# Kernel tuning notes

Hardware: AMD Instinct MI355X
Metric: run time of the kernel (lower is better)

The kernel has to match this reference:

```python
import jax, jax.numpy as jnp
import numpy as np
import math

B, NMAX, PE, E, DS, NF = 8, 128, 64, 5, 64, 8  # E = num_edge_features + 1


def setup_inputs() -> dict:
    key = jax.random.key(0)
    ks = jax.random.split(key, 10)
    total = B * NMAX
    x = jax.random.normal(ks[0], (total, PE), jnp.float32)
    batch = jnp.arange(total, dtype=jnp.int32) // NMAX  # sorted graph ids, full graphs
    q = jax.random.uniform(ks[1], (B,), jnp.float32, 0.1, 0.9)  # keep sin(2*pi*q) away from 0
    s = 0.05
    return dict(
        x=x, batch=batch, q=q,
        w_attn=jax.random.normal(ks[2], (PE, 4 * E * PE), jnp.float32) * s,
        b_attn=jnp.zeros((4 * E * PE,), jnp.float32),
        w_node=jax.random.normal(ks[3], (PE, NF), jnp.float32) * s,
        b_node=jnp.zeros((NF,), jnp.float32),
        w_phi=jax.random.normal(ks[4], (DS,), jnp.float32) * s,   # Linear(1, DS) weight
        b_phi=jax.random.normal(ks[5], (DS,), jnp.float32) * s,
        w_ctx=jax.random.normal(ks[6], (DS, DS), jnp.float32) * s,  # Linear(DS, DS, bias=False)
        w_self=jax.random.normal(ks[7], (DS,), jnp.float32) * s,  # Linear(1, DS) weight
        b_self=jax.random.normal(ks[8], (DS,), jnp.float32) * s,
        w_out=jax.random.normal(ks[9], (DS,), jnp.float32) * s,   # Linear(DS, 1) weight
        b_out=jnp.zeros((), jnp.float32),
    )


def _to_dense(batch, vals, n_graphs, n_max):
    # torch_geometric.to_dense_batch for sorted batch vector
    starts = jnp.searchsorted(batch, jnp.arange(n_graphs, dtype=batch.dtype))
    pos = jnp.arange(batch.shape[0]) - starts[batch]
    dense = jnp.zeros((n_graphs, n_max, vals.shape[-1]), vals.dtype).at[batch, pos].set(vals)
    mask = jnp.zeros((n_graphs, n_max), bool).at[batch, pos].set(True)
    return dense, mask


def reference(x, batch, q, w_attn, b_attn, w_node, b_node,
              w_phi, b_phi, w_ctx, w_self, b_self, w_out, b_out):
    scale = 1.0 / math.sqrt(E * PE)
    x_hat = x @ w_node + b_node                              # (total, NF)
    proj = x @ w_attn + b_attn                               # (total, 4*E*PE)
    dense, mask = _to_dense(batch, proj, B, NMAX)            # (B, N, 4*E*PE), (B, N)
    k1, q1, k2, q2 = jnp.split(dense, 4, axis=-1)
    heads = lambda t: t.reshape(B, NMAX, E, PE).transpose(0, 2, 1, 3)  # (B, E, N, PE)
    k1, q1, k2, q2 = heads(k1), heads(q1), heads(k2), heads(q2)
    z_re = jnp.einsum('bend,bemd->benm', k1, q1) * scale     # (B, E, N, N)
    z_im = jnp.einsum('bend,bemd->benm', k2, q2) * scale
    c = jnp.cos(2.0 * math.pi * q)[:, None, None, None]
    s = jnp.sin(2.0 * math.pi * q)[:, None, None, None]
    z = z_re + z_im * (2.0 - c) / s                          # (B, E, N, N)
    eye = jnp.eye(NMAX, dtype=bool)
    edge_mask = mask[:, :, None] & mask[:, None, :] & ~eye   # (B, N, N)
    # DeepSetClassifier
    zt = z[..., None]                                        # (B, E, N, N, 1)
    phi_out = zt * w_phi + b_phi                             # (B, E, N, N, DS)
    m = edge_mask[:, None, :, :, None].astype(z.dtype)       # (B, 1, N, N, 1)
    denom = jnp.maximum(edge_mask.sum(-1).astype(z.dtype), 1.0)[:, None, :, None]  # (B,1,N,1)
    ctx = (m * phi_out).sum(3) / denom                       # (B, E, N, DS) masked neighbor mean
    h = jax.nn.gelu(zt * w_self + b_self + (ctx @ w_ctx)[:, :, :, None, :],
                    approximate=False)                        # (B, E, N, N, DS)
    e = (h * w_out).sum(-1) + b_out                          # (B, E, N, N)
    e_hat = jnp.transpose(e, (0, 3, 2, 1))                   # transpose(-1, 1) -> (B, N, N, E)
    return (e_hat, x_hat, edge_mask, mask)
```

## Files before the change

kernel.cpp:

```cpp
#include <hip/hip_runtime.h>
#include <hip/hip_bf16.h>

#define NB 8
#define NMAXN 128
#define PEH 64
#define NE 5
#define DSZ 64
#define NFEAT 8
#define TOTALN 1024
#define PCOLS 1280

#define OUT_XHAT (NB*NMAXN*NMAXN*NE)
#define OUT_EM   (OUT_XHAT + TOTALN*NFEAT)
#define OUT_MASK (OUT_EM + NB*NMAXN*NMAXN)


__global__ void k_fused1(const float* __restrict__ x, const float* __restrict__ qv,
                         const float* __restrict__ w_attn, const float* __restrict__ b_attn,
                         const float* __restrict__ w_node, const float* __restrict__ b_node,
                         const float* __restrict__ w_phi, const float* __restrict__ b_phi,
                         const float* __restrict__ w_ctx, const float* __restrict__ b_self,
                         float* __restrict__ ws, float* __restrict__ out,
                         int offZbar, int offWpc, int offC1, int offFac, int doProj)
{
    int blk = blockIdx.x, t = threadIdx.x;
    if (blk < 256) {
        if (!doProj) return;
        __shared__ float xs[4 * 64];
        int r0 = blk * 4;
        if (t < 256) xs[t] = x[r0 * PEH + t];
        __syncthreads();
        float4 b4 = *(const float4*)&b_attn[4 * t];
        float4 a0 = b4, a1 = b4, a2 = b4, a3 = b4;
        const float* wp = w_attn + 4 * t;
        #pragma unroll 4
        for (int k = 0; k < 64; k++) {
            float4 w4 = *(const float4*)&wp[k * PCOLS];
            float x0 = xs[k], x1 = xs[64 + k], x2 = xs[128 + k], x3 = xs[192 + k];
            a0.x = fmaf(x0, w4.x, a0.x); a0.y = fmaf(x0, w4.y, a0.y); a0.z = fmaf(x0, w4.z, a0.z); a0.w = fmaf(x0, w4.w, a0.w);
            a1.x = fmaf(x1, w4.x, a1.x); a1.y = fmaf(x1, w4.y, a1.y); a1.z = fmaf(x1, w4.z, a1.z); a1.w = fmaf(x1, w4.w, a1.w);
            a2.x = fmaf(x2, w4.x, a2.x); a2.y = fmaf(x2, w4.y, a2.y); a2.z = fmaf(x2, w4.z, a2.z); a2.w = fmaf(x2, w4.w, a2.w);
            a3.x = fmaf(x3, w4.x, a3.x); a3.y = fmaf(x3, w4.y, a3.y); a3.z = fmaf(x3, w4.z, a3.z); a3.w = fmaf(x3, w4.w, a3.w);
        }
        float* pr = ws + r0 * PCOLS + 4 * t;
        *(float4*)&pr[0]         = a0;
        *(float4*)&pr[PCOLS]     = a1;
        *(float4*)&pr[2 * PCOLS] = a2;
        *(float4*)&pr[3 * PCOLS] = a3;
        return;
    }
    int b2 = blk - 256;
    if (b2 < 32) {
        if (t < 256) {
            int g = b2 * 256 + t;
            int row = g >> 3, f = g & 7;
            const float* xr = x + row * PEH;
            float acc = b_node[f];
            #pragma unroll 8
            for (int k = 0; k < PEH; k++) acc = fmaf(xr[k], w_node[k * NFEAT + f], acc);
            out[OUT_XHAT + g] = acc;
        }
    } else if (b2 < 48) {
        int base = (b2 - 32) * 8192;
        for (int g = base + t; g < base + 8192; g += 320) {
            int n = (g >> 7) & 127, m = g & 127;
            out[OUT_EM + g] = (n == m) ? 0.0f : 1.0f;
        }
    } else if (b2 == 48) {
        for (int g = t; g < 1024; g += 320) out[OUT_MASK + g] = 1.0f;
    } else if (b2 == 49) {
        if (t < 64) {
            float wpv = 0.f, bpv = 0.f;
            for (int i = 0; i < 64; i++) {
                float wc = w_ctx[i * 64 + t];
                wpv = fmaf(w_phi[i], wc, wpv);
                bpv = fmaf(b_phi[i], wc, bpv);
            }
            ws[offWpc + t] = wpv;
            ws[offC1 + t]  = b_self[t] + bpv;
        } else if (t < 72) {
            int b = t - 64;
            float qq = qv[b];
            float ang = 6.2831853071795864f * qq;
            float c = cosf(ang), s = sinf(ang);
            ws[offFac + b] = (2.0f - c) / s;
        }
    } else {
        int base = (b2 - 50) * 2560;
        for (int g = t; g < 2560; g += 320) ws[offZbar + base + g] = 0.0f;
    }
}

__device__ __forceinline__ void z_store4(float acc[4][4], float* ws, float* zp,
                                         int zsF, int offZbar,
                                         int b, int e, int mq, int t)
{
    int tx = t & 7, ty = t >> 3;
    int m0 = 4 * tx, n0 = 4 * ty;
    __hip_bfloat16* zsb = (__hip_bfloat16*)(ws + zsF);
    float psum[4] = {0.f, 0.f, 0.f, 0.f};
    #pragma unroll
    for (int c = 0; c < 4; c++) {
        int mg = mq * 32 + m0 + c;
        union { ushort4 u; __hip_bfloat16 h[4]; } pk;
        #pragma unroll
        for (int r = 0; r < 4; r++) {
            pk.h[r] = __float2bfloat16(acc[r][c]);
            if (mg != n0 + r) psum[r] += acc[r][c];
        }
        *(ushort4*)&zsb[((b * NMAXN + mg) * NE + e) * NMAXN + n0] = pk.u;
    }
    #pragma unroll
    for (int r = 0; r < 4; r++) zp[(n0 + r) * 8 + tx] = psum[r];
    __syncthreads();
    if (t < 128) {
        float s = 0.f;
        #pragma unroll
        for (int xx = 0; xx < 8; xx++) s += zp[t * 8 + xx];
        atomicAdd(&ws[offZbar + (b * NE + e) * NMAXN + t], s);
    }
}

__global__ void k_z_fast(float* __restrict__ ws, int zsF, int offZbar, int offFac)
{
    __shared__ alignas(16) float sm[8192 + 1280 + 1024];
    float* smA = sm;
    float* smQ = sm + 8192;
    float* zp  = sm + 8192 + 1280;

    int t = threadIdx.x;
    int blk = blockIdx.x;
    int ms = blk & 7, be = blk >> 3;
    int b = be / 5, e = be - 5 * b;
    float fac = ws[offFac + b];
    const float scale = 0.05590169943749474f;
    float sfac = scale * fac;

    const float* proj = ws;
    int kn = t >> 1, kkb = (t & 1) * 32;
    int qm = t & 15, qkb = (t >> 4) * 4;

    int tx = t & 7, ty = t >> 3;
    int m0 = 2 * tx, n0 = 4 * ty;
    float acc[4][2] = {};

    for (int pass = 0; pass < 2; pass++) {
        __syncthreads();
        int colK = (pass ? 640 : 0)   + e * 64;
        int colQ = (pass ? 960 : 320) + e * 64;
        float sc = pass ? sfac : scale;
        const float* prK = proj + (b * NMAXN + kn) * PCOLS + colK + kkb;
        #pragma unroll
        for (int j4 = 0; j4 < 8; j4++) {
            float4 v = *(const float4*)&prK[4 * j4];
            smA[(kkb + 4*j4 + 0) * 128 + kn] = sc * v.x;
            smA[(kkb + 4*j4 + 1) * 128 + kn] = sc * v.y;
            smA[(kkb + 4*j4 + 2) * 128 + kn] = sc * v.z;
            smA[(kkb + 4*j4 + 3) * 128 + kn] = sc * v.w;
        }
        const float* prQ = proj + (b * NMAXN + ms * 16 + qm) * PCOLS + colQ + qkb;
        {
            float4 v = *(const float4*)&prQ[0];
            smQ[(qkb + 0) * 20 + qm] = v.x;
            smQ[(qkb + 1) * 20 + qm] = v.y;
            smQ[(qkb + 2) * 20 + qm] = v.z;
            smQ[(qkb + 3) * 20 + qm] = v.w;
        }
        __syncthreads();
        for (int k = 0; k < 64; k++) {
            float4 a4 = *(const float4*)&smA[k * 128 + n0];
            float2 q2 = *(const float2*)&smQ[k * 20 + m0];
            float ar[4] = {a4.x, a4.y, a4.z, a4.w};
            #pragma unroll
            for (int r = 0; r < 4; r++) {
                acc[r][0] = fmaf(ar[r], q2.x, acc[r][0]);
                acc[r][1] = fmaf(ar[r], q2.y, acc[r][1]);
            }
        }
    }
    __syncthreads();

    __hip_bfloat16* zsb = (__hip_bfloat16*)(ws + zsF);
    float psum[4] = {0.f, 0.f, 0.f, 0.f};
    #pragma unroll
    for (int c = 0; c < 2; c++) {
        int mg = ms * 16 + m0 + c;
        union { ushort4 u; __hip_bfloat16 h[4]; } pk;
        #pragma unroll
        for (int r = 0; r < 4; r++) {
            pk.h[r] = __float2bfloat16(acc[r][c]);
            if (mg != n0 + r) psum[r] += acc[r][c];
        }
        *(ushort4*)&zsb[((b * NMAXN + mg) * NE + e) * NMAXN + n0] = pk.u;
    }
    #pragma unroll
    for (int r = 0; r < 4; r++) zp[(n0 + r) * 8 + tx] = psum[r];
    __syncthreads();
    if (t < 128) {
        float s = 0.f;
        #pragma unroll
        for (int xx = 0; xx < 8; xx++) s += zp[t * 8 + xx];
        atomicAdd(&ws[offZbar + (b * NE + e) * NMAXN + t], s);
    }
}

__global__ void k_z_slow(const float* __restrict__ x, const float* __restrict__ w_attn,
                         const float* __restrict__ b_attn, float* __restrict__ ws,
                         int zsF, int offZbar, int offFac)
{
    __shared__ alignas(16) float sm[8320 + 2304 + 1024];
    float* xsm = sm;
    float* smA = sm;
    float* smQ = sm + 8320;
    float* zp  = sm + 8320 + 2304;

    int t = threadIdx.x;
    int blk = blockIdx.x;
    int mq = blk & 3, be = blk >> 2;
    int b = be / 5, e = be - 5 * b;
    float fac = ws[offFac + b];
    const float scale = 0.05590169943749474f;
    float sfac = scale * fac;

    int kn   = t >> 1;
    int kkb  = (t & 1) * 32;
    int qm   = t & 31;
    int qkb  = (t >> 5) * 8;
    int mglo = mq * 32 + qm;

    int tx = t & 7, ty = t >> 3;
    int m0 = 4 * tx, n0 = 4 * ty;
    float acc[4][4] = {};

    for (int pass = 0; pass < 2; pass++) {
        __syncthreads();
        for (int i = t; i < 128 * 16; i += 256) {
            int n = i >> 4, dd = (i & 15) * 4;
            float4 xv = *(const float4*)&x[(b * NMAXN + n) * PEH + dd];
            float* dst = &xsm[n * 65 + dd];
            dst[0] = xv.x; dst[1] = xv.y; dst[2] = xv.z; dst[3] = xv.w;
        }
        __syncthreads();
        int colK = (pass ? 640 : 0)   + e * 64 + kkb;
        int colQ = (pass ? 960 : 320) + e * 64 + qkb;
        float rk[32], rq[8];
        #pragma unroll
        for (int j = 0; j < 32; j++) rk[j] = b_attn[colK + j];
        #pragma unroll
        for (int j = 0; j < 8; j++)  rq[j] = b_attn[colQ + j];
        for (int d = 0; d < 64; d++) {
            const float* wrow = w_attn + d * PCOLS;
            float xk = xsm[kn * 65 + d];
            float xq = xsm[mglo * 65 + d];
            #pragma unroll
            for (int j4 = 0; j4 < 8; j4++) {
                float4 w4 = *(const float4*)&wrow[colK + 4 * j4];
                rk[4*j4+0] = fmaf(xk, w4.x, rk[4*j4+0]);
                rk[4*j4+1] = fmaf(xk, w4.y, rk[4*j4+1]);
                rk[4*j4+2] = fmaf(xk, w4.z, rk[4*j4+2]);
                rk[4*j4+3] = fmaf(xk, w4.w, rk[4*j4+3]);
            }
            #pragma unroll
            for (int j4 = 0; j4 < 2; j4++) {
                float4 w4 = *(const float4*)&wrow[colQ + 4 * j4];
                rq[4*j4+0] = fmaf(xq, w4.x, rq[4*j4+0]);
                rq[4*j4+1] = fmaf(xq, w4.y, rq[4*j4+1]);
                rq[4*j4+2] = fmaf(xq, w4.z, rq[4*j4+2]);
                rq[4*j4+3] = fmaf(xq, w4.w, rq[4*j4+3]);
            }
        }
        __syncthreads();
        float sc = pass ? sfac : scale;
        #pragma unroll
        for (int j = 0; j < 32; j++) smA[(kkb + j) * 128 + kn] = sc * rk[j];
        #pragma unroll
        for (int j = 0; j < 8; j++)  smQ[(qkb + j) * 36 + qm] = rq[j];
        __syncthreads();
        for (int k = 0; k < 64; k++) {
            float4 a4 = *(const float4*)&smA[k * 128 + n0];
            float4 q4 = *(const float4*)&smQ[k * 36 + m0];
            float ar[4] = {a4.x, a4.y, a4.z, a4.w};
            float qr[4] = {q4.x, q4.y, q4.z, q4.w};
            #pragma unroll
            for (int r = 0; r < 4; r++)
                #pragma unroll
                for (int c = 0; c < 4; c++)
                    acc[r][c] = fmaf(ar[r], qr[c], acc[r][c]);
        }
    }
    __syncthreads();
    z_store4(acc, ws, zp, zsF, offZbar, b, e, mq, t);
}

__device__ __forceinline__ float gelu_fast(float x) {
    float x2 = x * x;
    float w  = -1.5957691216057308f * x * fmaf(0.044715f, x2, 1.0f);
    float ew = __expf(w);
    return x * __builtin_amdgcn_rcpf(1.0f + ew);
}

__global__ void k_epi(const float* __restrict__ ws, const float* __restrict__ w_self,
                      const float* __restrict__ w_out, const float* __restrict__ b_out,
                      float* __restrict__ out,
                      int zsF, int offZbar, int offWpc, int offC1)
{
    __shared__ alignas(16) float4 cwi[64];
    int t = threadIdx.x;
    int b = blockIdx.x >> 7, m = blockIdx.x & 127;
    if (t < 64)
        cwi[t] = make_float4(w_self[t], ws[offWpc + t], ws[offC1 + t], w_out[t]);
    float zbv = ws[offZbar + b * 640 + t] * (1.0f / 127.0f);
    __syncthreads();

    const __hip_bfloat16* zsb = (const __hip_bfloat16*)(ws + zsF);
    int e = t >> 7, n = t & 127;
    float zv = __bfloat162float(zsb[(b * NMAXN + m) * 640 + t]);
    float acc = b_out[0];
    #pragma unroll 8
    for (int d = 0; d < 64; d++) {
        float4 c = cwi[d];
        float arg = fmaf(zv, c.x, fmaf(zbv, c.y, c.z));
        acc = fmaf(gelu_fast(arg), c.w, acc);
    }
    out[(b * NMAXN + m) * 640 + n * NE + e] = acc;
}

extern "C" void kernel_launch(void* const* d_in, const int* in_sizes, int n_in,
                              void* d_out, int out_size, void* d_ws, size_t ws_size,
                              hipStream_t stream)
{
    const float* x      = (const float*)d_in[0];
    const float* q      = (const float*)d_in[2];
    const float* w_attn = (const float*)d_in[3];
    const float* b_attn = (const float*)d_in[4];
    const float* w_node = (const float*)d_in[5];
    const float* b_node = (const float*)d_in[6];
    const float* w_phi  = (const float*)d_in[7];
    const float* b_phi  = (const float*)d_in[8];
    const float* w_ctx  = (const float*)d_in[9];
    const float* w_self = (const float*)d_in[10];
    const float* b_self = (const float*)d_in[11];
    const float* w_out  = (const float*)d_in[12];
    const float* b_out  = (const float*)d_in[13];
    float* ws  = (float*)d_ws;
    float* out = (float*)d_out;

    const bool big = ws_size >= (size_t)(1643656 * 4 + 64);
    const int zsF     = big ? (TOTALN * PCOLS) : 0;
    const int offZbar = zsF + 327680;
    const int offWpc  = offZbar + 5120;
    const int offC1   = offWpc + 64;
    const int offFac  = offC1 + 64;

    k_fused1<<<308, 320, 0, stream>>>(x, q, w_attn, b_attn, w_node, b_node,
                                      w_phi, b_phi, w_ctx, b_self,
                                      ws, out, offZbar, offWpc, offC1, offFac, big ? 1 : 0);
    if (big) {
        k_z_fast<<<320, 256, 0, stream>>>(ws, zsF, offZbar, offFac);
    } else {
        k_z_slow<<<160, 256, 0, stream>>>(x, w_attn, b_attn, ws, zsF, offZbar, offFac);
    }
    k_epi<<<1024, 640, 0, stream>>>(ws, w_self, w_out, b_out, out,
                                    zsF, offZbar, offWpc, offC1);
}
```

Measured before the change: 120.6 us.

## Fuse z GEMM with GELU epilogue and compute neighbor sums algebraically

Replaces the z-GEMM kernel and the separate epilogue kernel with two kernels. The first computes each row's masked neighbor sum of z directly from the projections as k·(sum of Q minus own Q), so no atomics or stored z are needed. The second recomputes z tiles in registers and applies the GELU DeepSet epilogue in place, writing e_hat directly. This removes the bf16 z round trip through global memory and one launch. It adds an extra small launch and recomputes K tiles across more blocks.

```diff
diff --git a/kernel.cpp b/kernel.cpp
--- a/kernel.cpp
+++ b/kernel.cpp
@@ -91,6 +91,131 @@
     }
 }
 
+__global__ void k_qsum(float* __restrict__ ws, int offZbar, int offFac)
+{
+    __shared__ float Qs[128];
+    __shared__ float part[256];
+    int t = threadIdx.x, blk = blockIdx.x;
+    int b = blk / 5, e = blk - 5 * b;
+    float fac = ws[offFac + b];
+    const float scale = 0.05590169943749474f;
+    float sfac = scale * fac;
+    const float* proj = ws;
+
+    int grp = t >> 6, k = t & 63;
+    int colQ = ((grp >> 1) ? 960 : 320) + e * 64 + k;
+    int m0 = (grp & 1) * 64;
+    float s = 0.f;
+    for (int m = 0; m < 64; m++) s += proj[(b * NMAXN + m0 + m) * PCOLS + colQ];
+    part[t] = s;
+    __syncthreads();
+    if (t < 64)       Qs[t] = part[t] + part[t + 64];
+    else if (t < 128) Qs[t] = part[t + 64] + part[t + 128];
+    __syncthreads();
+
+    int n = t & 127, half = t >> 7;
+    int colK  = (half ? 640 : 0)   + e * 64;
+    int colQ2 = (half ? 960 : 320) + e * 64;
+    const float* rowp = proj + (b * NMAXN + n) * PCOLS;
+    float sc = half ? sfac : scale;
+    float d = 0.f;
+    #pragma unroll 4
+    for (int kk = 0; kk < 64; kk++)
+        d += rowp[colK + kk] * (Qs[half * 64 + kk] - rowp[colQ2 + kk]);
+    part[t] = d * sc;
+    __syncthreads();
+    if (t < 128)
+        ws[offZbar + (b * NE + e) * NMAXN + t] = (part[t] + part[t + 128]) * (1.0f / 127.0f);
+}
+
+__device__ __forceinline__ float gelu_fast(float x) {
+    float x2 = x * x;
+    float w  = -1.5957691216057308f * x * fmaf(0.044715f, x2, 1.0f);
+    float ew = __expf(w);
+    return x * __builtin_amdgcn_rcpf(1.0f + ew);
+}
+
+__global__ void __launch_bounds__(256) k_zepi(float* __restrict__ ws,
+                      const float* __restrict__ w_self, const float* __restrict__ w_out,
+                      const float* __restrict__ b_out, float* __restrict__ out,
+                      int offZbar, int offWpc, int offC1, int offFac)
+{
+    __shared__ alignas(16) float smA[64 * 128];
+    __shared__ alignas(16) float smQ[64 * 12];
+    __shared__ alignas(16) float zbs[128];
+    __shared__ alignas(16) float4 cwi[64];
+
+    int t = threadIdx.x, blk = blockIdx.x;
+    int ms = blk & 15, be = blk >> 4;
+    int b = be / 5, e = be - 5 * b;
+    float fac = ws[offFac + b];
+    const float scale = 0.05590169943749474f;
+    float sfac = scale * fac;
+    const float* proj = ws;
+
+    if (t < 64)  cwi[t] = make_float4(w_self[t], ws[offWpc + t], ws[offC1 + t], w_out[t]);
+    if (t < 128) zbs[t] = ws[offZbar + (b * NE + e) * NMAXN + t];
+
+    int kn = t >> 1, kkb = (t & 1) * 32;
+    int qm = t & 7,  qkb = (t >> 3) * 2;
+    int tx = t & 7,  ty = t >> 3;
+    int n0 = 4 * ty;
+    int mg = ms * 8 + tx;
+    float acc[4] = {0.f, 0.f, 0.f, 0.f};
+
+    for (int pass = 0; pass < 2; pass++) {
+        __syncthreads();
+        int colK = (pass ? 640 : 0)   + e * 64;
+        int colQ = (pass ? 960 : 320) + e * 64;
+        float sc = pass ? sfac : scale;
+        const float* prK = proj + (b * NMAXN + kn) * PCOLS + colK + kkb;
+        #pragma unroll
+        for (int j4 = 0; j4 < 8; j4++) {
+            float4 v = *(const float4*)&prK[4 * j4];
+            smA[(kkb + 4*j4 + 0) * 128 + kn] = sc * v.x;
+            smA[(kkb + 4*j4 + 1) * 128 + kn] = sc * v.y;
+            smA[(kkb + 4*j4 + 2) * 128 + kn] = sc * v.z;
+            smA[(kkb + 4*j4 + 3) * 128 + kn] = sc * v.w;
+        }
+        {
+            float2 v = *(const float2*)&proj[(b * NMAXN + mg) * PCOLS + colQ + qkb];
+            smQ[(qkb + 0) * 12 + qm] = v.x;
+            smQ[(qkb + 1) * 12 + qm] = v.y;
+        }
+        __syncthreads();
+        #pragma unroll 4
+        for (int k = 0; k < 64; k++) {
+            const float4 a4 = *(const float4*)&smA[k * 128 + n0];
+            float qv = smQ[k * 12 + tx];
+            acc[0] = fmaf(a4.x, qv, acc[0]);
+            acc[1] = fmaf(a4.y, qv, acc[1]);
+            acc[2] = fmaf(a4.z, qv, acc[2]);
+            acc[3] = fmaf(a4.w, qv, acc[3]);
+        }
+    }
+
+    float zb0 = zbs[n0], zb1 = zbs[n0 + 1], zb2 = zbs[n0 + 2], zb3 = zbs[n0 + 3];
+    float bo = b_out[0];
+    float e0 = bo, e1 = bo, e2 = bo, e3 = bo;
+    #pragma unroll 4
+    for (int d = 0; d < 64; d++) {
+        float4 c = cwi[d];
+        float a0 = fmaf(acc[0], c.x, fmaf(zb0, c.y, c.z));
+        float a1 = fmaf(acc[1], c.x, fmaf(zb1, c.y, c.z));
+        float a2 = fmaf(acc[2], c.x, fmaf(zb2, c.y, c.z));
+        float a3 = fmaf(acc[3], c.x, fmaf(zb3, c.y, c.z));
+        e0 = fmaf(gelu_fast(a0), c.w, e0);
+        e1 = fmaf(gelu_fast(a1), c.w, e1);
+        e2 = fmaf(gelu_fast(a2), c.w, e2);
+        e3 = fmaf(gelu_fast(a3), c.w, e3);
+    }
+    float* op = out + ((size_t)(b * NMAXN + mg) * NMAXN + n0) * NE + e;
+    op[0]      = e0;
+    op[NE]     = e1;
+    op[2 * NE] = e2;
+    op[3 * NE] = e3;
+}
+
 __device__ __forceinline__ void z_store4(float acc[4][4], float* ws, float* zp,
                                          int zsF, int offZbar,
                                          int b, int e, int mq, int t)
@@ -102,89 +227,6 @@
     #pragma unroll
     for (int c = 0; c < 4; c++) {
         int mg = mq * 32 + m0 + c;
-        union { ushort4 u; __hip_bfloat16 h[4]; } pk;
-        #pragma unroll
-        for (int r = 0; r < 4; r++) {
-            pk.h[r] = __float2bfloat16(acc[r][c]);
-            if (mg != n0 + r) psum[r] += acc[r][c];
-        }
-        *(ushort4*)&zsb[((b * NMAXN + mg) * NE + e) * NMAXN + n0] = pk.u;
-    }
-    #pragma unroll
-    for (int r = 0; r < 4; r++) zp[(n0 + r) * 8 + tx] = psum[r];
-    __syncthreads();
-    if (t < 128) {
-        float s = 0.f;
-        #pragma unroll
-        for (int xx = 0; xx < 8; xx++) s += zp[t * 8 + xx];
-        atomicAdd(&ws[offZbar + (b * NE + e) * NMAXN + t], s);
-    }
-}
-
-__global__ void k_z_fast(float* __restrict__ ws, int zsF, int offZbar, int offFac)
-{
-    __shared__ alignas(16) float sm[8192 + 1280 + 1024];
-    float* smA = sm;
-    float* smQ = sm + 8192;
-    float* zp  = sm + 8192 + 1280;
-
-    int t = threadIdx.x;
-    int blk = blockIdx.x;
-    int ms = blk & 7, be = blk >> 3;
-    int b = be / 5, e = be - 5 * b;
-    float fac = ws[offFac + b];
-    const float scale = 0.05590169943749474f;
-    float sfac = scale * fac;
-
-    const float* proj = ws;
-    int kn = t >> 1, kkb = (t & 1) * 32;
-    int qm = t & 15, qkb = (t >> 4) * 4;
-
-    int tx = t & 7, ty = t >> 3;
-    int m0 = 2 * tx, n0 = 4 * ty;
-    float acc[4][2] = {};
-
-    for (int pass = 0; pass < 2; pass++) {
-        __syncthreads();
-        int colK = (pass ? 640 : 0)   + e * 64;
-        int colQ = (pass ? 960 : 320) + e * 64;
-        float sc = pass ? sfac : scale;
-        const float* prK = proj + (b * NMAXN + kn) * PCOLS + colK + kkb;
-        #pragma unroll
-        for (int j4 = 0; j4 < 8; j4++) {
-            float4 v = *(const float4*)&prK[4 * j4];
-            smA[(kkb + 4*j4 + 0) * 128 + kn] = sc * v.x;
-            smA[(kkb + 4*j4 + 1) * 128 + kn] = sc * v.y;
-            smA[(kkb + 4*j4 + 2) * 128 + kn] = sc * v.z;
-            smA[(kkb + 4*j4 + 3) * 128 + kn] = sc * v.w;
-        }
-        const float* prQ = proj + (b * NMAXN + ms * 16 + qm) * PCOLS + colQ + qkb;
-        {
-            float4 v = *(const float4*)&prQ[0];
-            smQ[(qkb + 0) * 20 + qm] = v.x;
-            smQ[(qkb + 1) * 20 + qm] = v.y;
-            smQ[(qkb + 2) * 20 + qm] = v.z;
-            smQ[(qkb + 3) * 20 + qm] = v.w;
-        }
-        __syncthreads();
-        for (int k = 0; k < 64; k++) {
-            float4 a4 = *(const float4*)&smA[k * 128 + n0];
-            float2 q2 = *(const float2*)&smQ[k * 20 + m0];
-            float ar[4] = {a4.x, a4.y, a4.z, a4.w};
-            #pragma unroll
-            for (int r = 0; r < 4; r++) {
-                acc[r][0] = fmaf(ar[r], q2.x, acc[r][0]);
-                acc[r][1] = fmaf(ar[r], q2.y, acc[r][1]);
-            }
-        }
-    }
-    __syncthreads();
-
-    __hip_bfloat16* zsb = (__hip_bfloat16*)(ws + zsF);
-    float psum[4] = {0.f, 0.f, 0.f, 0.f};
-    #pragma unroll
-    for (int c = 0; c < 2; c++) {
-        int mg = ms * 16 + m0 + c;
         union { ushort4 u; __hip_bfloat16 h[4]; } pk;
         #pragma unroll
         for (int r = 0; r < 4; r++) {
@@ -292,13 +334,6 @@
     z_store4(acc, ws, zp, zsF, offZbar, b, e, mq, t);
 }
 
-__device__ __forceinline__ float gelu_fast(float x) {
-    float x2 = x * x;
-    float w  = -1.5957691216057308f * x * fmaf(0.044715f, x2, 1.0f);
-    float ew = __expf(w);
-    return x * __builtin_amdgcn_rcpf(1.0f + ew);
-}
-
 __global__ void k_epi(const float* __restrict__ ws, const float* __restrict__ w_self,
                       const float* __restrict__ w_out, const float* __restrict__ b_out,
                       float* __restrict__ out,
@@ -356,10 +391,12 @@
                                       w_phi, b_phi, w_ctx, b_self,
                                       ws, out, offZbar, offWpc, offC1, offFac, big ? 1 : 0);
     if (big) {
-        k_z_fast<<<320, 256, 0, stream>>>(ws, zsF, offZbar, offFac);
+        k_qsum<<<40, 256, 0, stream>>>(ws, offZbar, offFac);
+        k_zepi<<<640, 256, 0, stream>>>(ws, w_self, w_out, b_out, out,
+                                        offZbar, offWpc, offC1, offFac);
     } else {
         k_z_slow<<<160, 256, 0, stream>>>(x, w_attn, b_attn, ws, zsF, offZbar, offFac);
-    }
-    k_epi<<<1024, 640, 0, stream>>>(ws, w_self, w_out, b_out, out,
-                                    zsF, offZbar, offWpc, offC1);
-}
+        k_epi<<<1024, 640, 0, stream>>>(ws, w_self, w_out, b_out, out,
+                                        zsF, offZbar, offWpc, offC1);
+    }
+}
```

Measured after the change: 127.8 us. 6.0% more time.

## Fuse z computation with GELU epilogue and compute neighbor mean algebraically

Applied to the files above, without the earlier changes.

Replaces the separate z kernel and epilogue kernel on the fast path with one kernel. It computes the z tile in registers and applies the DeepSet GELU epilogue directly, so the bf16 z buffer round trip and the atomic zbar accumulation go away. The masked neighbor mean is computed per block as K·(sum of Q minus own Q), which uses the linearity of the dot product. Every block recomputes the full 128-row zbar and the Q column sums, which adds redundant loads and FMA work. Output stores are strided by NE, so they are uncoalesced.

```diff
diff --git a/kernel.cpp b/kernel.cpp
--- a/kernel.cpp
+++ b/kernel.cpp
@@ -9,6 +9,7 @@
 #define NFEAT 8
 #define TOTALN 1024
 #define PCOLS 1280
+#define SQS 130
 
 #define OUT_XHAT (NB*NMAXN*NMAXN*NE)
 #define OUT_EM   (OUT_XHAT + TOTALN*NFEAT)
@@ -91,6 +92,121 @@
     }
 }
 
+__device__ __forceinline__ float gelu_fast(float x) {
+    float x2 = x * x;
+    float w  = -1.5957691216057308f * x * fmaf(0.044715f, x2, 1.0f);
+    float ew = __expf(w);
+    return x * __builtin_amdgcn_rcpf(1.0f + ew);
+}
+
+__global__ void __launch_bounds__(256) k_zepi(float* __restrict__ ws,
+                      const float* __restrict__ w_self, const float* __restrict__ w_out,
+                      const float* __restrict__ b_out, float* __restrict__ out,
+                      int offWpc, int offC1, int offFac)
+{
+    __shared__ alignas(16) float smA[64 * 128];
+    __shared__ alignas(16) float smQ[64 * SQS];
+    __shared__ float qpart[256];
+    __shared__ float Qs[64];
+    __shared__ float zbs[128];
+    __shared__ alignas(16) float4 cwi[64];
+
+    int t = threadIdx.x, blk = blockIdx.x;
+    int ms = blk & 7, be = blk >> 3;
+    int b = be / 5, e = be - 5 * b;
+    float fac = ws[offFac + b];
+    const float scale = 0.05590169943749474f;
+    float sfac = scale * fac;
+    const float* proj = ws;
+
+    if (t < 64) cwi[t] = make_float4(w_self[t], ws[offWpc + t], ws[offC1 + t], w_out[t]);
+
+    int kn = t >> 1, kkb = (t & 1) * 32;
+    int qk = t & 63, qmq = t >> 6;
+    int tx = t & 7, ty = t >> 3;
+    int n0 = 4 * ty;
+    int mg = ms * 16 + 2 * tx;
+
+    float acc[4][2] = {};
+    float zb_acc = 0.f;
+
+    for (int pass = 0; pass < 2; pass++) {
+        __syncthreads();
+        int colK = (pass ? 640 : 0)   + e * 64;
+        int colQ = (pass ? 960 : 320) + e * 64;
+        float sc = pass ? sfac : scale;
+        const float* prK = proj + (b * NMAXN + kn) * PCOLS + colK + kkb;
+        const float* prQ = proj + (b * NMAXN + kn) * PCOLS + colQ + kkb;
+        #pragma unroll
+        for (int j4 = 0; j4 < 8; j4++) {
+            float4 v = *(const float4*)&prK[4 * j4];
+            smA[(kkb + 4*j4 + 0) * 128 + kn] = sc * v.x;
+            smA[(kkb + 4*j4 + 1) * 128 + kn] = sc * v.y;
+            smA[(kkb + 4*j4 + 2) * 128 + kn] = sc * v.z;
+            smA[(kkb + 4*j4 + 3) * 128 + kn] = sc * v.w;
+            float4 u = *(const float4*)&prQ[4 * j4];
+            smQ[(kkb + 4*j4 + 0) * SQS + kn] = u.x;
+            smQ[(kkb + 4*j4 + 1) * SQS + kn] = u.y;
+            smQ[(kkb + 4*j4 + 2) * SQS + kn] = u.z;
+            smQ[(kkb + 4*j4 + 3) * SQS + kn] = u.w;
+        }
+        {
+            const float* qcol = proj + (b * NMAXN + qmq * 32) * PCOLS + colQ + qk;
+            float s = 0.f;
+            #pragma unroll 4
+            for (int mm = 0; mm < 32; mm++) s += qcol[mm * PCOLS];
+            qpart[t] = s;
+        }
+        __syncthreads();
+        if (t < 64) Qs[t] = (qpart[t] + qpart[t + 64]) + (qpart[t + 128] + qpart[t + 192]);
+        __syncthreads();
+        if (t < 128) {
+            float d = 0.f;
+            #pragma unroll 4
+            for (int k = 0; k < 64; k++) {
+                float a = smA[k * 128 + t];
+                d = fmaf(a, Qs[k] - smQ[k * SQS + t], d);
+            }
+            zb_acc += d;
+        }
+        #pragma unroll 4
+        for (int k = 0; k < 64; k++) {
+            const float4 a4 = *(const float4*)&smA[k * 128 + n0];
+            float q0 = smQ[k * SQS + mg];
+            float q1 = smQ[k * SQS + mg + 1];
+            acc[0][0] = fmaf(a4.x, q0, acc[0][0]); acc[0][1] = fmaf(a4.x, q1, acc[0][1]);
+            acc[1][0] = fmaf(a4.y, q0, acc[1][0]); acc[1][1] = fmaf(a4.y, q1, acc[1][1]);
+            acc[2][0] = fmaf(a4.z, q0, acc[2][0]); acc[2][1] = fmaf(a4.z, q1, acc[2][1]);
+            acc[3][0] = fmaf(a4.w, q0, acc[3][0]); acc[3][1] = fmaf(a4.w, q1, acc[3][1]);
+        }
+    }
+    if (t < 128) zbs[t] = zb_acc * (1.0f / 127.0f);
+    __syncthreads();
+
+    float zb0 = zbs[n0], zb1 = zbs[n0 + 1], zb2 = zbs[n0 + 2], zb3 = zbs[n0 + 3];
+    float bo = b_out[0];
+    float e00 = bo, e10 = bo, e20 = bo, e30 = bo;
+    float e01 = bo, e11 = bo, e21 = bo, e31 = bo;
+    #pragma unroll 4
+    for (int d = 0; d < 64; d++) {
+        float4 c = cwi[d];
+        float z0 = fmaf(zb0, c.y, c.z), z1 = fmaf(zb1, c.y, c.z);
+        float z2 = fmaf(zb2, c.y, c.z), z3 = fmaf(zb3, c.y, c.z);
+        e00 = fmaf(gelu_fast(fmaf(acc[0][0], c.x, z0)), c.w, e00);
+        e10 = fmaf(gelu_fast(fmaf(acc[1][0], c.x, z1)), c.w, e10);
+        e20 = fmaf(gelu_fast(fmaf(acc[2][0], c.x, z2)), c.w, e20);
+        e30 = fmaf(gelu_fast(fmaf(acc[3][0], c.x, z3)), c.w, e30);
+        e01 = fmaf(gelu_fast(fmaf(acc[0][1], c.x, z0)), c.w, e01);
+        e11 = fmaf(gelu_fast(fmaf(acc[1][1], c.x, z1)), c.w, e11);
+        e21 = fmaf(gelu_fast(fmaf(acc[2][1], c.x, z2)), c.w, e21);
+        e31 = fmaf(gelu_fast(fmaf(acc[3][1], c.x, z3)), c.w, e31);
+    }
+    float* op0 = out + ((size_t)(b * NMAXN + mg) * NMAXN + n0) * NE + e;
+    float* op1 = op0 + (size_t)NMAXN * NE;
+    op0[0] = e00; op0[NE] = e10; op0[2*NE] = e20; op0[3*NE] = e30;
+    op1[0] = e01; op1[NE] = e11; op1[2*NE] = e21; op1[3*NE] = e31;
+}
+
 __device__ __forceinline__ void z_store4(float acc[4][4], float* ws, float* zp,
                                          int zsF, int offZbar,
                                          int b, int e, int mq, int t)
@@ -102,89 +218,6 @@
     #pragma unroll
     for (int c = 0; c < 4; c++) {
         int mg = mq * 32 + m0 + c;
-        union { ushort4 u; __hip_bfloat16 h[4]; } pk;
-        #pragma unroll
-        for (int r = 0; r < 4; r++) {
-            pk.h[r] = __float2bfloat16(acc[r][c]);
-            if (mg != n0 + r) psum[r] += acc[r][c];
-        }
-        *(ushort4*)&zsb[((b * NMAXN + mg) * NE + e) * NMAXN + n0] = pk.u;
-    }
-    #pragma unroll
-    for (int r = 0; r < 4; r++) zp[(n0 + r) * 8 + tx] = psum[r];
-    __syncthreads();
-    if (t < 128) {
-        float s = 0.f;
-        #pragma unroll
-        for (int xx = 0; xx < 8; xx++) s += zp[t * 8 + xx];
-        atomicAdd(&ws[offZbar + (b * NE + e) * NMAXN + t], s);
-    }
-}
-
-__global__ void k_z_fast(float* __restrict__ ws, int zsF, int offZbar, int offFac)
-{
-    __shared__ alignas(16) float sm[8192 + 1280 + 1024];
-    float* smA = sm;
-    float* smQ = sm + 8192;
-    float* zp  = sm + 8192 + 1280;
-
-    int t = threadIdx.x;
-    int blk = blockIdx.x;
-    int ms = blk & 7, be = blk >> 3;
-    int b = be / 5, e = be - 5 * b;
-    float fac = ws[offFac + b];
-    const float scale = 0.05590169943749474f;
-    float sfac = scale * fac;
-
-    const float* proj = ws;
-    int kn = t >> 1, kkb = (t & 1) * 32;
-    int qm = t & 15, qkb = (t >> 4) * 4;
-
-    int tx = t & 7, ty = t >> 3;
-    int m0 = 2 * tx, n0 = 4 * ty;
-    float acc[4][2] = {};
-
-    for (int pass = 0; pass < 2; pass++) {
-        __syncthreads();
-        int colK = (pass ? 640 : 0)   + e * 64;
-        int colQ = (pass ? 960 : 320) + e * 64;
-        float sc = pass ? sfac : scale;
-        const float* prK = proj + (b * NMAXN + kn) * PCOLS + colK + kkb;
-        #pragma unroll
-        for (int j4 = 0; j4 < 8; j4++) {
-            float4 v = *(const float4*)&prK[4 * j4];
-            smA[(kkb + 4*j4 + 0) * 128 + kn] = sc * v.x;
-            smA[(kkb + 4*j4 + 1) * 128 + kn] = sc * v.y;
-            smA[(kkb + 4*j4 + 2) * 128 + kn] = sc * v.z;
-            smA[(kkb + 4*j4 + 3) * 128 + kn] = sc * v.w;
-        }
-        const float* prQ = proj + (b * NMAXN + ms * 16 + qm) * PCOLS + colQ + qkb;
-        {
-            float4 v = *(const float4*)&prQ[0];
-            smQ[(qkb + 0) * 20 + qm] = v.x;
-            smQ[(qkb + 1) * 20 + qm] = v.y;
-            smQ[(qkb + 2) * 20 + qm] = v.z;
-            smQ[(qkb + 3) * 20 + qm] = v.w;
-        }
-        __syncthreads();
-        for (int k = 0; k < 64; k++) {
-            float4 a4 = *(const float4*)&smA[k * 128 + n0];
-            float2 q2 = *(const float2*)&smQ[k * 20 + m0];
-            float ar[4] = {a4.x, a4.y, a4.z, a4.w};
-            #pragma unroll
-            for (int r = 0; r < 4; r++) {
-                acc[r][0] = fmaf(ar[r], q2.x, acc[r][0]);
-                acc[r][1] = fmaf(ar[r], q2.y, acc[r][1]);
-            }
-        }
-    }
-    __syncthreads();
-
-    __hip_bfloat16* zsb = (__hip_bfloat16*)(ws + zsF);
-    float psum[4] = {0.f, 0.f, 0.f, 0.f};
-    #pragma unroll
-    for (int c = 0; c < 2; c++) {
-        int mg = ms * 16 + m0 + c;
         union { ushort4 u; __hip_bfloat16 h[4]; } pk;
         #pragma unroll
         for (int r = 0; r < 4; r++) {
@@ -292,13 +325,6 @@
     z_store4(acc, ws, zp, zsF, offZbar, b, e, mq, t);
 }
 
-__device__ __forceinline__ float gelu_fast(float x) {
-    float x2 = x * x;
-    float w  = -1.5957691216057308f * x * fmaf(0.044715f, x2, 1.0f);
-    float ew = __expf(w);
-    return x * __builtin_amdgcn_rcpf(1.0f + ew);
-}
-
 __global__ void k_epi(const float* __restrict__ ws, const float* __restrict__ w_self,
                       const float* __restrict__ w_out, const float* __restrict__ b_out,
                       float* __restrict__ out,
@@ -356,10 +382,11 @@
                                       w_phi, b_phi, w_ctx, b_self,
                                       ws, out, offZbar, offWpc, offC1, offFac, big ? 1 : 0);
     if (big) {
-        k_z_fast<<<320, 256, 0, stream>>>(ws, zsF, offZbar, offFac);
+        k_zepi<<<320, 256, 0, stream>>>(ws, w_self, w_out, b_out, out,
+                                        offWpc, offC1, offFac);
     } else {
         k_z_slow<<<160, 256, 0, stream>>>(x, w_attn, b_attn, ws, zsF, offZbar, offFac);
-    }
-    k_epi<<<1024, 640, 0, stream>>>(ws, w_self, w_out, b_out, out,
-                                    zsF, offZbar, offWpc, offC1);
-}
+        k_epi<<<1024, 640, 0, stream>>>(ws, w_self, w_out, b_out, out,
+                                        zsF, offZbar, offWpc, offC1);
+    }
+}
```

After: 133.9 us. 1.11x slower.
